# Optimization experiments

Measured on AMD Instinct MI355X. Metric: run time of the kernel, lower is better.

Reference implementation:

```python
import jax, jax.numpy as jnp
import numpy as np

BATCH = 16384
MAX_ACTIVE = 32
FEAT = 768
HIDDEN = 1024


def setup_inputs() -> dict:
    key = jax.random.key(0)
    k1, k2, k3, k4, k5, k6 = jax.random.split(key, 6)
    stm = jax.random.randint(k1, (BATCH, MAX_ACTIVE), 0, FEAT, dtype=jnp.int32)
    nstm = jax.random.randint(k2, (BATCH, MAX_ACTIVE), 0, FEAT, dtype=jnp.int32)
    # Linear params (PyTorch layout: weight is (out_features, in_features))
    ft_w = jax.random.normal(k3, (HIDDEN, FEAT), dtype=jnp.float32) * 0.05
    ft_b = jax.random.normal(k4, (HIDDEN,), dtype=jnp.float32) * 0.05
    out_w = jax.random.normal(k5, (1, 2 * HIDDEN), dtype=jnp.float32) * 0.05
    out_b = jax.random.normal(k6, (1,), dtype=jnp.float32) * 0.05
    return {"stm": stm, "nstm": nstm, "ft_w": ft_w, "ft_b": ft_b,
            "out_w": out_w, "out_b": out_b}


def sparse_to_dense(indices: jnp.ndarray, size: int = FEAT) -> jnp.ndarray:
    """(B, max_active) int indices with -1 padding -> (B, size) 0/1 float32."""
    b = indices.shape[0]
    valid = (indices >= 0).astype(jnp.float32)          # (B, A)
    cols = jnp.clip(indices, 0, size - 1)               # padded -> col 0, masked by `valid`
    rows = jnp.arange(b, dtype=jnp.int32)[:, None]      # (B, 1) broadcast
    dense = jnp.zeros((b, size), dtype=jnp.float32)
    # .max matches torch's set-to-1 semantics even if duplicate indices occur
    return dense.at[rows, cols].max(valid)


def reference(stm, nstm, ft_w, ft_b, out_w, out_b):
    stm_d = sparse_to_dense(stm)                        # (B, 768)
    nstm_d = sparse_to_dense(nstm)                      # (B, 768)
    stm_h = stm_d @ ft_w.T + ft_b                       # (B, H)
    nstm_h = nstm_d @ ft_w.T + ft_b                     # (B, H)
    hidden = jnp.concatenate([stm_h, nstm_h], axis=1)   # (B, 2H)
    hidden = jnp.clip(hidden, 0.0, 1.0)
    return jax.nn.sigmoid(hidden @ out_w.T + out_b)     # (B, 1)
```

## Files before the change

### kernel.cpp

```cpp
#include <hip/hip_runtime.h>
#include <hip/hip_bf16.h>
#include <stdint.h>

#define BATCH 16384
#define MAXA 32
#define FEAT 768
#define HIDDEN 1024

__global__ __launch_bounds__(768) void quantize_ft(const float* __restrict__ ftw,
                                                   uint8_t* __restrict__ wQ,
                                                   float* __restrict__ scale) {
  const int h = blockIdx.x;
  const int f = threadIdx.x;
  const float w = ftw[h * FEAT + f];
  float a = fabsf(w);
#pragma unroll
  for (int off = 32; off > 0; off >>= 1)
    a = fmaxf(a, __shfl_xor(a, off, 64));
  __shared__ float red[12];
  __shared__ float inv_sh;
  if ((threadIdx.x & 63) == 0) red[threadIdx.x >> 6] = a;
  __syncthreads();
  if (threadIdx.x == 0) {
    float m = red[0];
#pragma unroll
    for (int i = 1; i < 12; ++i) m = fmaxf(m, red[i]);
    m = fmaxf(m, 1e-20f);
    scale[h] = m / 127.f;
    inv_sh = 127.f / m;
  }
  __syncthreads();
  int q = __float2int_rn(w * inv_sh);
  wQ[(size_t)f * HIDDEN + h] = (uint8_t)(q + 128);
}

__device__ __forceinline__ void acc16(uint32_t* acc, uint4 w) {
  acc[0] += __builtin_amdgcn_perm(0u, w.x, 0x0c010c00u);
  acc[1] += __builtin_amdgcn_perm(0u, w.x, 0x0c030c02u);
  acc[2] += __builtin_amdgcn_perm(0u, w.y, 0x0c010c00u);
  acc[3] += __builtin_amdgcn_perm(0u, w.y, 0x0c030c02u);
  acc[4] += __builtin_amdgcn_perm(0u, w.z, 0x0c010c00u);
  acc[5] += __builtin_amdgcn_perm(0u, w.z, 0x0c030c02u);
  acc[6] += __builtin_amdgcn_perm(0u, w.w, 0x0c010c00u);
  acc[7] += __builtin_amdgcn_perm(0u, w.w, 0x0c030c02u);
}

__global__ __launch_bounds__(256) void nn_fwd(
    const int* __restrict__ stm, const int* __restrict__ nstm,
    const uint8_t* __restrict__ wQ, const float* __restrict__ scale,
    const float* __restrict__ bias, const float* __restrict__ outw,
    const float* __restrict__ outb, float* __restrict__ out)
{
  const int lane = threadIdx.x & 63;
  const int row  = blockIdx.x * 4 + (threadIdx.x >> 6);
  const int half = lane >> 5;
  const int pos  = lane & 31;

  const int* __restrict__ src = half ? nstm : stm;
  int idx = src[row * MAXA + pos];
  bool valid = idx >= 0;
#pragma unroll
  for (int j = 0; j < 31; ++j) {
    int other = __shfl(idx, (half << 5) | j, 64);
    if (j < pos && other == idx) valid = false;
  }
  const uint64_t mask = __ballot(valid);

  uint32_t accs[8], accn[8];
#pragma unroll
  for (int k = 0; k < 8; ++k) { accs[k] = 0u; accn[k] = 0u; }

  const uint8_t* wbase = wQ + (size_t)lane * 16;

  {
    uint32_t ms = (uint32_t)(mask & 0xffffffffull);
    while (ms) {
      int j0 = __builtin_ctz(ms); ms &= ms - 1;
      int f0 = __builtin_amdgcn_readlane(idx, j0);
      const uint4* p0 = (const uint4*)(wbase + (size_t)f0 * HIDDEN);
      if (ms) {
        int j1 = __builtin_ctz(ms); ms &= ms - 1;
        int f1 = __builtin_amdgcn_readlane(idx, j1);
        const uint4* p1 = (const uint4*)(wbase + (size_t)f1 * HIDDEN);
        uint4 w0 = *p0;
        uint4 w1 = *p1;
        acc16(accs, w0);
        acc16(accs, w1);
      } else {
        acc16(accs, *p0);
      }
    }
  }
  {
    uint32_t ms = (uint32_t)(mask >> 32);
    while (ms) {
      int j0 = __builtin_ctz(ms); ms &= ms - 1;
      int f0 = __builtin_amdgcn_readlane(idx, 32 + j0);
      const uint4* p0 = (const uint4*)(wbase + (size_t)f0 * HIDDEN);
      if (ms) {
        int j1 = __builtin_ctz(ms); ms &= ms - 1;
        int f1 = __builtin_amdgcn_readlane(idx, 32 + j1);
        const uint4* p1 = (const uint4*)(wbase + (size_t)f1 * HIDDEN);
        uint4 w0 = *p0;
        uint4 w1 = *p1;
        acc16(accn, w0);
        acc16(accn, w1);
      } else {
        acc16(accn, *p0);
      }
    }
  }

  const int bs = 128 * __builtin_popcountll(mask & 0xffffffffull);
  const int bn = 128 * __builtin_popcountll(mask >> 32);

  const int hbase = lane * 16;
  float sc[16], bb[16], ows[16], own[16];
  {
    const float4* s4 = (const float4*)(scale + hbase);
    const float4* b4 = (const float4*)(bias + hbase);
    const float4* oS = (const float4*)(outw + hbase);
    const float4* oN = (const float4*)(outw + HIDDEN + hbase);
#pragma unroll
    for (int q = 0; q < 4; ++q) {
      float4 v;
      v = s4[q]; sc[4*q]=v.x; sc[4*q+1]=v.y; sc[4*q+2]=v.z; sc[4*q+3]=v.w;
      v = b4[q]; bb[4*q]=v.x; bb[4*q+1]=v.y; bb[4*q+2]=v.z; bb[4*q+3]=v.w;
      v = oS[q]; ows[4*q]=v.x; ows[4*q+1]=v.y; ows[4*q+2]=v.z; ows[4*q+3]=v.w;
      v = oN[q]; own[4*q]=v.x; own[4*q+1]=v.y; own[4*q+2]=v.z; own[4*q+3]=v.w;
    }
  }
  float partial = 0.f;
#pragma unroll
  for (int k = 0; k < 16; ++k) {
    uint32_t as = accs[k >> 1], an = accn[k >> 1];
    int qs = (int)((k & 1) ? (as >> 16) : (as & 0xffffu)) - bs;
    int qn = (int)((k & 1) ? (an >> 16) : (an & 0xffffu)) - bn;
    float hs = fminf(fmaxf(fmaf((float)qs, sc[k], bb[k]), 0.f), 1.f);
    float hn = fminf(fmaxf(fmaf((float)qn, sc[k], bb[k]), 0.f), 1.f);
    partial += hs * ows[k] + hn * own[k];
  }
#pragma unroll
  for (int off = 32; off > 0; off >>= 1)
    partial += __shfl_down(partial, off, 64);
  if (lane == 0) {
    float y = partial + outb[0];
    out[row] = 1.f / (1.f + __expf(-y));
  }
}

extern "C" void kernel_launch(void* const* d_in, const int* in_sizes, int n_in,
                              void* d_out, int out_size, void* d_ws, size_t ws_size,
                              hipStream_t stream) {
  const int*   stm  = (const int*)d_in[0];
  const int*   nstm = (const int*)d_in[1];
  const float* ftw  = (const float*)d_in[2];
  const float* ftb  = (const float*)d_in[3];
  const float* outw = (const float*)d_in[4];
  const float* outb = (const float*)d_in[5];

  uint8_t* wQ    = (uint8_t*)d_ws;
  float*   scale = (float*)((uint8_t*)d_ws + (size_t)FEAT * HIDDEN);

  quantize_ft<<<HIDDEN, FEAT, 0, stream>>>(ftw, wQ, scale);
  nn_fwd<<<BATCH / 4, 256, 0, stream>>>(stm, nstm, wQ, scale, ftb, outw, outb,
                                        (float*)d_out);
}
```

Measured before the change: 124.3 us.

## Tile the weight quantize transpose and fully unroll the gather with a padded zero row

The single quantize kernel, which wrote transposed bytes with fully uncoalesced stores, is split into a per-row scale kernel and a 64x64 tiled quantize-transpose that stages through shared memory and writes 16-byte coalesced rows. A sentinel row of 0x80 bytes (quantized zero) is appended, so invalid or duplicate features map to it. The gather loop then becomes a fixed 32-iteration unrolled loop with no ballot or ctz branching, and it uses a constant bias correction. This adds an extra launch and always performs 32 loads per side, but all of them can be issued back to back.

```diff
diff --git a/kernel.cpp b/kernel.cpp
--- a/kernel.cpp
+++ b/kernel.cpp
@@ -7,31 +7,58 @@
 #define FEAT 768
 #define HIDDEN 1024
 
-__global__ __launch_bounds__(768) void quantize_ft(const float* __restrict__ ftw,
-                                                   uint8_t* __restrict__ wQ,
-                                                   float* __restrict__ scale) {
+__global__ __launch_bounds__(256) void scale_k(const float* __restrict__ ftw,
+                                               float* __restrict__ scale,
+                                               float* __restrict__ invsc,
+                                               uint8_t* __restrict__ wQ) {
+  if (blockIdx.x == HIDDEN) {
+    if (threadIdx.x < 64) {
+      uint4 v; v.x = v.y = v.z = v.w = 0x80808080u;
+      ((uint4*)(wQ + (size_t)FEAT * HIDDEN))[threadIdx.x] = v;
+    }
+    return;
+  }
   const int h = blockIdx.x;
-  const int f = threadIdx.x;
-  const float w = ftw[h * FEAT + f];
-  float a = fabsf(w);
+  float a = 0.f;
+#pragma unroll
+  for (int p = 0; p < 3; ++p)
+    a = fmaxf(a, fabsf(ftw[h * FEAT + p * 256 + threadIdx.x]));
 #pragma unroll
   for (int off = 32; off > 0; off >>= 1)
     a = fmaxf(a, __shfl_xor(a, off, 64));
-  __shared__ float red[12];
-  __shared__ float inv_sh;
+  __shared__ float red[4];
   if ((threadIdx.x & 63) == 0) red[threadIdx.x >> 6] = a;
   __syncthreads();
   if (threadIdx.x == 0) {
-    float m = red[0];
-#pragma unroll
-    for (int i = 1; i < 12; ++i) m = fmaxf(m, red[i]);
+    float m = fmaxf(fmaxf(red[0], red[1]), fmaxf(red[2], red[3]));
     m = fmaxf(m, 1e-20f);
     scale[h] = m / 127.f;
-    inv_sh = 127.f / m;
+    invsc[h] = 127.f / m;
+  }
+}
+
+__global__ __launch_bounds__(256) void tilequant(const float* __restrict__ ftw,
+                                                 const float* __restrict__ invsc,
+                                                 uint8_t* __restrict__ wQ) {
+  const int f0 = (blockIdx.x % (FEAT / 64)) * 64;
+  const int h0 = (blockIdx.x / (FEAT / 64)) * 64;
+  __shared__ uint8_t tile[64][80];
+  __shared__ float inv[64];
+  if (threadIdx.x < 64) inv[threadIdx.x] = invsc[h0 + threadIdx.x];
+  __syncthreads();
+  const int ff = threadIdx.x & 63;
+  const int hb = threadIdx.x >> 6;
+#pragma unroll
+  for (int p = 0; p < 16; ++p) {
+    int hh = p * 4 + hb;
+    float w = ftw[(size_t)(h0 + hh) * FEAT + f0 + ff];
+    int q = __float2int_rn(w * inv[hh]);
+    tile[ff][hh] = (uint8_t)(q + 128);
   }
   __syncthreads();
-  int q = __float2int_rn(w * inv_sh);
-  wQ[(size_t)f * HIDDEN + h] = (uint8_t)(q + 128);
+  const int fs = threadIdx.x >> 2, part = threadIdx.x & 3;
+  uint4 v = *(const uint4*)&tile[fs][part * 16];
+  *(uint4*)(wQ + (size_t)(f0 + fs) * HIDDEN + h0 + part * 16) = v;
 }
 
 __device__ __forceinline__ void acc16(uint32_t* acc, uint4 w) {
@@ -64,55 +91,25 @@
     int other = __shfl(idx, (half << 5) | j, 64);
     if (j < pos && other == idx) valid = false;
   }
-  const uint64_t mask = __ballot(valid);
+  const int fmap = valid ? idx : FEAT;
 
   uint32_t accs[8], accn[8];
 #pragma unroll
   for (int k = 0; k < 8; ++k) { accs[k] = 0u; accn[k] = 0u; }
 
-  const uint8_t* wbase = wQ + (size_t)lane * 16;
-
-  {
-    uint32_t ms = (uint32_t)(mask & 0xffffffffull);
-    while (ms) {
-      int j0 = __builtin_ctz(ms); ms &= ms - 1;
-      int f0 = __builtin_amdgcn_readlane(idx, j0);
-      const uint4* p0 = (const uint4*)(wbase + (size_t)f0 * HIDDEN);
-      if (ms) {
-        int j1 = __builtin_ctz(ms); ms &= ms - 1;
-        int f1 = __builtin_amdgcn_readlane(idx, j1);
-        const uint4* p1 = (const uint4*)(wbase + (size_t)f1 * HIDDEN);
-        uint4 w0 = *p0;
-        uint4 w1 = *p1;
-        acc16(accs, w0);
-        acc16(accs, w1);
-      } else {
-        acc16(accs, *p0);
-      }
-    }
-  }
-  {
-    uint32_t ms = (uint32_t)(mask >> 32);
-    while (ms) {
-      int j0 = __builtin_ctz(ms); ms &= ms - 1;
-      int f0 = __builtin_amdgcn_readlane(idx, 32 + j0);
-      const uint4* p0 = (const uint4*)(wbase + (size_t)f0 * HIDDEN);
-      if (ms) {
-        int j1 = __builtin_ctz(ms); ms &= ms - 1;
-        int f1 = __builtin_amdgcn_readlane(idx, 32 + j1);
-        const uint4* p1 = (const uint4*)(wbase + (size_t)f1 * HIDDEN);
-        uint4 w0 = *p0;
-        uint4 w1 = *p1;
-        acc16(accn, w0);
-        acc16(accn, w1);
-      } else {
-        acc16(accn, *p0);
-      }
-    }
+#pragma unroll
+  for (int j = 0; j < 32; ++j) {
+    int fs_ = __builtin_amdgcn_readlane(fmap, j);
+    int fn_ = __builtin_amdgcn_readlane(fmap, 32 + j);
+    const uint4* ps = (const uint4*)(wQ + (size_t)fs_ * HIDDEN);
+    const uint4* pn = (const uint4*)(wQ + (size_t)fn_ * HIDDEN);
+    uint4 ws_ = ps[lane];
+    uint4 wn_ = pn[lane];
+    acc16(accs, ws_);
+    acc16(accn, wn_);
   }
 
-  const int bs = 128 * __builtin_popcountll(mask & 0xffffffffull);
-  const int bn = 128 * __builtin_popcountll(mask >> 32);
+  const int DB = 32 * 128;
 
   const int hbase = lane * 16;
   float sc[16], bb[16], ows[16], own[16];
@@ -134,8 +131,8 @@
 #pragma unroll
   for (int k = 0; k < 16; ++k) {
     uint32_t as = accs[k >> 1], an = accn[k >> 1];
-    int qs = (int)((k & 1) ? (as >> 16) : (as & 0xffffu)) - bs;
-    int qn = (int)((k & 1) ? (an >> 16) : (an & 0xffffu)) - bn;
+    int qs = (int)((k & 1) ? (as >> 16) : (as & 0xffffu)) - DB;
+    int qn = (int)((k & 1) ? (an >> 16) : (an & 0xffffu)) - DB;
     float hs = fminf(fmaxf(fmaf((float)qs, sc[k], bb[k]), 0.f), 1.f);
     float hn = fminf(fmaxf(fmaf((float)qn, sc[k], bb[k]), 0.f), 1.f);
     partial += hs * ows[k] + hn * own[k];
@@ -160,9 +157,11 @@
   const float* outb = (const float*)d_in[5];
 
   uint8_t* wQ    = (uint8_t*)d_ws;
-  float*   scale = (float*)((uint8_t*)d_ws + (size_t)FEAT * HIDDEN);
+  float*   scale = (float*)(wQ + (size_t)(FEAT + 1) * HIDDEN);
+  float*   invsc = scale + HIDDEN;
 
-  quantize_ft<<<HIDDEN, FEAT, 0, stream>>>(ftw, wQ, scale);
+  scale_k<<<HIDDEN + 1, 256, 0, stream>>>(ftw, scale, invsc, wQ);
+  tilequant<<<(FEAT / 64) * (HIDDEN / 64), 256, 0, stream>>>(ftw, invsc, wQ);
   nn_fwd<<<BATCH / 4, 256, 0, stream>>>(stm, nstm, wQ, scale, ftb, outw, outb,
                                         (float*)d_out);
 }
```

New measurement: 120.1 us. -3.3%, faster.
